# Optimization experiments

Hardware: AMD Instinct MI355X
Metric: run time of the kernel (lower is better)

## Reference

```python
import jax, jax.numpy as jnp
import numpy as np

H = 16  # num_attention_heads

def setup_inputs() -> dict:
    key = jax.random.key(0)
    ks = jax.random.split(key, 4)
    B, S, D = 4, 2048, 1024
    scale = 1.0 / np.sqrt(D)
    return {
        "hidden_states": jax.random.normal(ks[0], (B, S, D), dtype=jnp.float32),
        "attention_mask": jnp.zeros((B, 1, 1, S), dtype=jnp.float32),
        "Wq": jax.random.normal(ks[1], (D, D), dtype=jnp.float32) * scale,
        "bq": jnp.zeros((D,), dtype=jnp.float32),
        "Wk": jax.random.normal(ks[2], (D, D), dtype=jnp.float32) * scale,
        "bk": jnp.zeros((D,), dtype=jnp.float32),
        "Wv": jax.random.normal(ks[3], (D, D), dtype=jnp.float32) * scale,
        "bv": jnp.zeros((D,), dtype=jnp.float32),
    }

def _split_heads(x, B, S):
    # [B,S,D] -> [B,H,S,Dh]
    return x.reshape(B, S, H, -1).transpose(0, 2, 1, 3)

def reference(hidden_states, attention_mask, Wq, bq, Wk, bk, Wv, bv):
    B, S, D = hidden_states.shape
    Dh = D // H
    q = _split_heads(hidden_states @ Wq.T + bq, B, S)  # [B,H,S,Dh]
    k = _split_heads(hidden_states @ Wk.T + bk, B, S)
    v = _split_heads(hidden_states @ Wv.T + bv, B, S)
    scores = jnp.einsum("bhqd,bhkd->bhqk", q, k) / jnp.sqrt(jnp.float32(Dh))
    scores = scores + attention_mask  # additive mask, broadcast [B,1,1,S]
    probs = jax.nn.softmax(scores, axis=-1)  # dropout is identity in eval mode
    ctx = jnp.einsum("bhqk,bhkd->bhqd", probs, v)  # [B,H,S,Dh]
    ctx = ctx.transpose(0, 2, 1, 3).reshape(B, S, D)
    return ctx
```

## Files before the change

### kernel.cpp

```cpp
#include <hip/hip_runtime.h>
#include <hip/hip_bf16.h>
#include <stdint.h>

#define LOG2E 1.44269504088896340736f
#define SCL   (0.125f * LOG2E)

typedef __attribute__((ext_vector_type(8)))  short short8;
typedef __attribute__((ext_vector_type(16))) float floatx16;
typedef __attribute__((ext_vector_type(4)))  unsigned short ushort4v;

#define GLP(g, l)                                                              \
    __builtin_amdgcn_global_load_lds(                                          \
        (const __attribute__((address_space(1))) void*)(g),                    \
        (__attribute__((address_space(3))) void*)(l), 16, 0, 0)

#if __has_builtin(__builtin_amdgcn_exp2f)
#define EXP2(x) __builtin_amdgcn_exp2f(x)
#else
#define EXP2(x) exp2f(x)
#endif

static __device__ __forceinline__ unsigned short f2bf(float f) {
    union { float f; unsigned u; } v; v.f = f;
    unsigned r = v.u + 0x7FFFu + ((v.u >> 16) & 1u);
    return (unsigned short)(r >> 16);
}

static __device__ __forceinline__ unsigned pack2bf(float a, float b) {
    __hip_bfloat162 h = __float22bfloat162_rn(make_float2(a, b));
    union { __hip_bfloat162 h; unsigned u; } c; c.h = h; return c.u;
}

#define EXPPACK(dst, sv, base) do {                                            \
        float p0 = EXP2((sv)[(base) + 0]), p1 = EXP2((sv)[(base) + 1]);        \
        float p2 = EXP2((sv)[(base) + 2]), p3 = EXP2((sv)[(base) + 3]);        \
        float p4 = EXP2((sv)[(base) + 4]), p5 = EXP2((sv)[(base) + 5]);        \
        float p6 = EXP2((sv)[(base) + 6]), p7 = EXP2((sv)[(base) + 7]);        \
        dst.uu[0] = pack2bf(p0, p1); dst.uu[1] = pack2bf(p2, p3);              \
        dst.uu[2] = pack2bf(p4, p5); dst.uu[3] = pack2bf(p6, p7);              \
    } while (0)

__global__ __launch_bounds__(256) void cvt_all(const float* __restrict__ X,
                                               const float* __restrict__ Wq,
                                               const float* __restrict__ Wk,
                                               const float* __restrict__ Wv,
                                               const float* __restrict__ mask,
                                               unsigned short* __restrict__ xb,
                                               unsigned short* __restrict__ wb,
                                               float* __restrict__ maskl) {
    int i = blockIdx.x * 256 + threadIdx.x;
    if (i < 2097152) {
        float4 v = ((const float4*)X)[i];
        ushort4v o;
        o.x = f2bf(v.x); o.y = f2bf(v.y); o.z = f2bf(v.z); o.w = f2bf(v.w);
        ((ushort4v*)xb)[i] = o;
    } else if (i < 2883584) {
        int j = i - 2097152;
        const float* src; int k;
        if (j < 262144)      { src = Wq; k = j; }
        else if (j < 524288) { src = Wk; k = j - 262144; }
        else                 { src = Wv; k = j - 524288; }
        float4 v = ((const float4*)src)[k];
        ushort4v o;
        o.x = f2bf(v.x); o.y = f2bf(v.y); o.z = f2bf(v.z); o.w = f2bf(v.w);
        ((ushort4v*)wb)[j] = o;
    } else if (i < 2883584 + 2048) {
        int j = i - 2883584;
        float4 v = ((const float4*)mask)[j];
        ((float4*)maskl)[j] = make_float4(v.x * LOG2E, v.y * LOG2E,
                                          v.z * LOG2E, v.w * LOG2E);
    }
}

__global__ __launch_bounds__(512)
__attribute__((amdgpu_waves_per_eu(2, 2))) void qkv_gemm(
        const unsigned short* __restrict__ X,
        const unsigned short* __restrict__ W,
        const float* __restrict__ bq, const float* __restrict__ bk,
        const float* __restrict__ bv,
        unsigned short* __restrict__ Qf,
        unsigned short* __restrict__ Kf,
        unsigned short* __restrict__ Vt)
{
    __shared__ __align__(16) unsigned short AB[65536];

    const int tid  = threadIdx.x;
    const int lane = tid & 63;
    const int wv   = tid >> 6;
    const int q32  = lane & 31;
    const int hi   = lane >> 5;
    const int sw   = q32 & 7;
    const int mBase = blockIdx.x * 256;
    const int nBase = blockIdx.y * 256;
    const int wm = (wv >> 2) * 128;
    const int wn = (wv & 3) * 64;

    floatx16 acc[4][2];
#pragma unroll
    for (int mi = 0; mi < 4; ++mi) { acc[mi][0] = 0.0f; acc[mi][1] = 0.0f; }

    const int sr = lane >> 3;
    const int kc = (lane & 7) ^ sr;

    const unsigned short* aBase[4];
    const unsigned short* bBase[4];
#pragma unroll
    for (int ks = 0; ks < 4; ++ks) {
        const int cs = ((2 * ks + hi) ^ sw) * 8;
        aBase[ks] = AB + ((wv >> 2) * 16 + (q32 >> 3)) * 512 + sw * 64 + cs;
        bBase[ks] = AB + 32768 + ((wv & 3) * 8 + (q32 >> 3)) * 512 + sw * 64 + cs;
    }

    auto STAGE = [&](int kb, int so) {
#pragma unroll
        for (int r = 0; r < 4; ++r) {
            const int seg = r * 8 + wv;
            const int row = seg * 8 + sr;
            GLP(X + (size_t)(mBase + row) * 1024 + kb + kc * 8, AB + so + seg * 512);
            GLP(W + (size_t)(nBase + row) * 1024 + kb + kc * 8, AB + 32768 + so + seg * 512);
        }
    };

    STAGE(0, 0);
    asm volatile("s_waitcnt vmcnt(0)" ::: "memory");
    __builtin_amdgcn_s_barrier();

#pragma unroll 1
    for (int t = 0; t < 16; ++t) {
        const int so  = (t & 1) * 16384;
        if (t < 15) STAGE((t + 1) * 64, ((t + 1) & 1) * 16384);
        short8 bF[2][4];
#pragma unroll
        for (int ni = 0; ni < 2; ++ni)
#pragma unroll
            for (int ks = 0; ks < 4; ++ks)
                bF[ni][ks] = *(const short8*)(bBase[ks] + so + ni * 2048);
#pragma unroll
        for (int mi = 0; mi < 4; ++mi) {
            short8 aF[4];
#pragma unroll
            for (int ks = 0; ks < 4; ++ks)
                aF[ks] = *(const short8*)(aBase[ks] + so + mi * 2048);
#pragma unroll
            for (int ks = 0; ks < 4; ++ks) {
                acc[mi][0] = __builtin_amdgcn_mfma_f32_32x32x16_bf16(
                    aF[ks], bF[0][ks], acc[mi][0], 0, 0, 0);
                acc[mi][1] = __builtin_amdgcn_mfma_f32_32x32x16_bf16(
                    aF[ks], bF[1][ks], acc[mi][1], 0, 0, 0);
            }
        }
        asm volatile("s_waitcnt vmcnt(0) lgkmcnt(0)" ::: "memory");
        __builtin_amdgcn_s_barrier();
    }

    if (blockIdx.y < 8) {
        unsigned short* dst = (blockIdx.y < 4) ? Qf : Kf;
        const float* bias   = (blockIdx.y < 4) ? bq : bk;
        const float scl     = (blockIdx.y < 4) ? SCL : 1.0f;
        const int nb = nBase & 1023;
        float bj[2];
#pragma unroll
        for (int ni = 0; ni < 2; ++ni)
            bj[ni] = bias[nb + wn + ni * 32 + q32];
#pragma unroll 1
        for (int hh = 0; hh < 2; ++hh) {
            if ((wm >> 7) == hh) {
#pragma unroll
                for (int ni = 0; ni < 2; ++ni) {
                    const int col = wn + ni * 32 + q32;
#pragma unroll
                    for (int mi = 0; mi < 4; ++mi)
#pragma unroll
                        for (int g = 0; g < 4; ++g) {
                            const int row0 = mi * 32 + g * 8 + hi * 4;
#pragma unroll
                            for (int rr = 0; rr < 4; ++rr)
                                AB[(row0 + rr) * 264 + col] =
                                    f2bf((acc[mi][ni][g * 4 + rr] + bj[ni]) * scl);
                        }
                }
            }
            __syncthreads();
#pragma unroll
            for (int it = 0; it < 8; ++it) {
                const int row  = it * 16 + (tid >> 5);
                const int part = tid & 31;
                short8 v = *(const short8*)(AB + row * 264 + part * 8);
                *(short8*)(dst + (size_t)(mBase + hh * 128 + row) * 1024
                               + nb + part * 8) = v;
            }
            __syncthreads();
        }
    } else {
#pragma unroll
        for (int ni = 0; ni < 2; ++ni) {
            const int c = (nBase - 2048) + wn + ni * 32 + q32;
            const int h = c >> 6;
            const int d = c & 63;
            const float bias = bv[c];
#pragma unroll
            for (int mi = 0; mi < 4; ++mi)
#pragma unroll
                for (int g = 0; g < 4; ++g) {
                    const int m0 = mBase + wm + mi * 32 + g * 8 + hi * 4;
                    const int b  = m0 >> 11;
                    const int s0 = m0 & 2047;
                    const int sp = (s0 & ~12) | ((s0 & 4) << 1) | ((s0 & 8) >> 1);
                    ushort4v pv;
#pragma unroll
                    for (int rr = 0; rr < 4; ++rr)
                        pv[rr] = f2bf(acc[mi][ni][g * 4 + rr] + bias);
                    *(ushort4v*)(Vt + (size_t)((b * 16 + h) * 64 + d) * 2048 + sp) = pv;
                }
        }
    }
}

__global__ __launch_bounds__(256)
__attribute__((amdgpu_waves_per_eu(2, 2))) void attn_kernel(
        const unsigned short* __restrict__ Qf,
        const unsigned short* __restrict__ Kf,
        const unsigned short* __restrict__ VT,
        const float* __restrict__ maskl,
        float* __restrict__ out)
{
    __shared__ __align__(16) unsigned short Ksh[2 * 128 * 64];
    __shared__ __align__(16) unsigned short Vsh[2 * 64 * 128];
    __shared__ __align__(16) float Mall[2048];

    const int tid  = threadIdx.x;
    const int lane = tid & 63;
    const int wv   = tid >> 6;
    const int q32  = lane & 31;
    const int hi   = lane >> 5;
    const int bh   = blockIdx.x & 63;
    const int qt   = blockIdx.x >> 6;
    const int b    = bh >> 4;
    const int h    = bh & 15;
    const int q0   = qt * 256 + wv * 64;
    const int sw   = q32 & 7;

    short8 bQ0[4], bQ1[4];
#pragma unroll
    for (int ks = 0; ks < 4; ++ks) {
        bQ0[ks] = *(const short8*)(Qf + (size_t)(b * 2048 + q0 + q32) * 1024
                                      + h * 64 + ks * 16 + hi * 8);
        bQ1[ks] = *(const short8*)(Qf + (size_t)(b * 2048 + q0 + 32 + q32) * 1024
                                      + h * 64 + ks * 16 + hi * 8);
    }

    short8 ones;
#pragma unroll
    for (int j = 0; j < 8; ++j) ones[j] = (short)0x3F80;

    floatx16 accO00 = 0.0f, accO01 = 0.0f;
    floatx16 accO10 = 0.0f, accO11 = 0.0f;
    floatx16 lacc0 = 0.0f, lacc1 = 0.0f;

    const unsigned short* gK = Kf + (size_t)(b * 2048) * 1024 + h * 64;
    const unsigned short* gV = VT + (size_t)(bh * 64) * 2048;
    const float* mrow = maskl + b * 2048;

    const unsigned short* kb4[4];
    const unsigned short* vb4[4];
#pragma unroll
    for (int ks = 0; ks < 4; ++ks) {
        const int cs = (2 * ks + hi) ^ sw;
        kb4[ks] = Ksh + q32 * 64 + cs * 8;
        vb4[ks] = Vsh + q32 * 128 + cs * 8;
    }

    const int krr = lane >> 3;
    const int kcs = lane & 7;
    const int vrr = lane >> 4;
    const int vcs = lane & 15;

    auto STAGE = [&](int kbn, int so) {
#pragma unroll
        for (int s = 0; s < 4; ++s) {
            const int seg = wv * 4 + s;
            const int rK  = seg * 8 + krr;
            const int cK  = kcs ^ (rK & 7);
            GLP(gK + (size_t)(kbn + rK) * 1024 + cK * 8, Ksh + so + seg * 512);
            const int rV  = seg * 4 + vrr;
            const int cV  = vcs ^ (rV & 7);
            GLP(gV + (size_t)rV * 2048 + kbn + cV * 8, Vsh + so + seg * 512);
        }
    };

    auto TILE = [&](int kb, int ro, int so) {
        if (kb + 128 < 2048) STAGE(kb + 128, so);
        const float* mloc = Mall + kb + hi * 4;
#pragma unroll 1
        for (int half = 0; half < 2; ++half) {
            short8 aK0[4], aK1[4];
#pragma unroll
            for (int ks = 0; ks < 4; ++ks) {
                aK0[ks] = *(const short8*)(kb4[ks] + ro + half * 4096);
                aK1[ks] = *(const short8*)(kb4[ks] + ro + half * 4096 + 2048);
            }
            const float* mh = mloc + half * 64;
#pragma unroll
            for (int mt = 0; mt < 2; ++mt) {
                const short8* aK = (mt == 0) ? aK0 : aK1;
                floatx16 mC;
#pragma unroll
                for (int a = 0; a < 4; ++a) {
                    float4 mv = *(const float4*)(mh + mt * 32 + a * 8);
                    mC[4 * a + 0] = mv.x; mC[4 * a + 1] = mv.y;
                    mC[4 * a + 2] = mv.z; mC[4 * a + 3] = mv.w;
                }
                __builtin_amdgcn_s_setprio(1);
                floatx16 s0 = __builtin_amdgcn_mfma_f32_32x32x16_bf16(aK[0], bQ0[0], mC, 0, 0, 0);
                floatx16 s1 = __builtin_amdgcn_mfma_f32_32x32x16_bf16(aK[0], bQ1[0], mC, 0, 0, 0);
#pragma unroll
                for (int ks = 1; ks < 4; ++ks) {
                    s0 = __builtin_amdgcn_mfma_f32_32x32x16_bf16(aK[ks], bQ0[ks], s0, 0, 0, 0);
                    s1 = __builtin_amdgcn_mfma_f32_32x32x16_bf16(aK[ks], bQ1[ks], s1, 0, 0, 0);
                }
                __builtin_amdgcn_s_setprio(0);
                short8 bVa0 = *(const short8*)(vb4[2 * mt + 0] + ro + half * 64);
                short8 bVa1 = *(const short8*)(vb4[2 * mt + 0] + ro + 4096 + half * 64);
                short8 bVb0 = *(const short8*)(vb4[2 * mt + 1] + ro + half * 64);
                short8 bVb1 = *(const short8*)(vb4[2 * mt + 1] + ro + 4096 + half * 64);
                union { unsigned uu[4]; short8 s; } aPa, aPb, aPc, aPd;
                EXPPACK(aPa, s0, 0);
                EXPPACK(aPb, s0, 8);
                EXPPACK(aPc, s1, 0);
                EXPPACK(aPd, s1, 8);
                __builtin_amdgcn_s_setprio(1);
                accO00 = __builtin_amdgcn_mfma_f32_32x32x16_bf16(aPa.s, bVa0, accO00, 0, 0, 0);
                accO01 = __builtin_amdgcn_mfma_f32_32x32x16_bf16(aPa.s, bVa1, accO01, 0, 0, 0);
                lacc0  = __builtin_amdgcn_mfma_f32_32x32x16_bf16(aPa.s, ones, lacc0, 0, 0, 0);
                accO00 = __builtin_amdgcn_mfma_f32_32x32x16_bf16(aPb.s, bVb0, accO00, 0, 0, 0);
                accO01 = __builtin_amdgcn_mfma_f32_32x32x16_bf16(aPb.s, bVb1, accO01, 0, 0, 0);
                lacc0  = __builtin_amdgcn_mfma_f32_32x32x16_bf16(aPb.s, ones, lacc0, 0, 0, 0);
                accO10 = __builtin_amdgcn_mfma_f32_32x32x16_bf16(aPc.s, bVa0, accO10, 0, 0, 0);
                accO11 = __builtin_amdgcn_mfma_f32_32x32x16_bf16(aPc.s, bVa1, accO11, 0, 0, 0);
                lacc1  = __builtin_amdgcn_mfma_f32_32x32x16_bf16(aPc.s, ones, lacc1, 0, 0, 0);
                accO10 = __builtin_amdgcn_mfma_f32_32x32x16_bf16(aPd.s, bVb0, accO10, 0, 0, 0);
                accO11 = __builtin_amdgcn_mfma_f32_32x32x16_bf16(aPd.s, bVb1, accO11, 0, 0, 0);
                lacc1  = __builtin_amdgcn_mfma_f32_32x32x16_bf16(aPd.s, ones, lacc1, 0, 0, 0);
                __builtin_amdgcn_s_setprio(0);
            }
        }
        asm volatile("s_waitcnt vmcnt(0) lgkmcnt(0)" ::: "memory");
        __builtin_amdgcn_s_barrier();
    };

#pragma unroll
    for (int s = 0; s < 2; ++s)
        GLP(mrow + (wv * 2 + s) * 256 + lane * 4, Mall + (wv * 2 + s) * 256);
    STAGE(0, 0);
    asm volatile("s_waitcnt vmcnt(0)" ::: "memory");
    __builtin_amdgcn_s_barrier();

#pragma unroll 1
    for (int kb2 = 0; kb2 < 2048; kb2 += 256) {
        TILE(kb2,       0,    8192);
        TILE(kb2 + 128, 8192, 0);
    }

#pragma unroll
    for (int g = 0; g < 4; ++g)
#pragma unroll
        for (int rr = 0; rr < 4; ++rr) {
            const int r   = g * 4 + rr;
            const int row = rr + 8 * g + 4 * hi;
            const float li0 = 1.0f / lacc0[r];
            const float li1 = 1.0f / lacc1[r];
            float* op0 = out + (size_t)(b * 2048 + q0 + row) * 1024 + h * 64 + q32;
            float* op1 = out + (size_t)(b * 2048 + q0 + 32 + row) * 1024 + h * 64 + q32;
            op0[0]  = accO00[r] * li0;
            op0[32] = accO01[r] * li0;
            op1[0]  = accO10[r] * li1;
            op1[32] = accO11[r] * li1;
        }
}

extern "C" void kernel_launch(void* const* d_in, const int* in_sizes, int n_in,
                              void* d_out, int out_size, void* d_ws, size_t ws_size,
                              hipStream_t stream) {
    const float* X    = (const float*)d_in[0];
    const float* mask = (const float*)d_in[1];
    const float* Wq   = (const float*)d_in[2];
    const float* bq   = (const float*)d_in[3];
    const float* Wk   = (const float*)d_in[4];
    const float* bk   = (const float*)d_in[5];
    const float* Wv   = (const float*)d_in[6];
    const float* bv   = (const float*)d_in[7];
    float* out = (float*)d_out;

    char* ws = (char*)d_ws;
    unsigned short* xb  = (unsigned short*)(ws);
    unsigned short* wb  = (unsigned short*)(ws + 16777216);
    unsigned short* qf  = (unsigned short*)(ws + 23068672);
    unsigned short* kf  = (unsigned short*)(ws + 39845888);
    unsigned short* vtb = (unsigned short*)(ws + 56623104);
    float*          ml  = (float*)(ws + 73400320);

    cvt_all<<<11272, 256, 0, stream>>>(X, Wq, Wk, Wv, mask, xb, wb, ml);

    qkv_gemm<<<dim3(32, 12), 512, 0, stream>>>(xb, wb, bq, bk, bv, qf, kf, vtb);

    attn_kernel<<<512, 256, 0, stream>>>(qf, kf, vtb, ml, out);
}
```

Before: 243.8 us.

## Software-pipeline QK MFMAs with exp and compute row sums on VALU

The attention inner tile is restructured into four phases. Each phase issues the QK^T MFMAs for the next 32-key subtile while exponentiating and packing the current scores, so matrix-core work overlaps the exp/pack VALU work. Row sums are now accumulated in fp32 on the VALU from the exponentials, then reduced across half-waves with a shuffle and passed through LDS. This replaces the extra MFMAs against a ones vector, removing a third of the PV-stage MFMAs. The cost is more live registers for the double-buffered score tiles and a normaliser summed from unrounded fp32 values instead of the bf16 values fed to the PV product.

After: 407.1 us. 1.67x slower.

```diff
diff --git a/kernel.cpp b/kernel.cpp
--- a/kernel.cpp
+++ b/kernel.cpp
@@ -31,11 +31,12 @@
     union { __hip_bfloat162 h; unsigned u; } c; c.h = h; return c.u;
 }
 
-#define EXPPACK(dst, sv, base) do {                                            \
+#define EXPPACKL(dst, sv, base, lacc) do {                                     \
         float p0 = EXP2((sv)[(base) + 0]), p1 = EXP2((sv)[(base) + 1]);        \
         float p2 = EXP2((sv)[(base) + 2]), p3 = EXP2((sv)[(base) + 3]);        \
         float p4 = EXP2((sv)[(base) + 4]), p5 = EXP2((sv)[(base) + 5]);        \
         float p6 = EXP2((sv)[(base) + 6]), p7 = EXP2((sv)[(base) + 7]);        \
+        lacc += ((p0 + p1) + (p2 + p3)) + ((p4 + p5) + (p6 + p7));             \
         dst.uu[0] = pack2bf(p0, p1); dst.uu[1] = pack2bf(p2, p3);              \
         dst.uu[2] = pack2bf(p4, p5); dst.uu[3] = pack2bf(p6, p7);              \
     } while (0)
@@ -227,6 +228,7 @@
     __shared__ __align__(16) unsigned short Ksh[2 * 128 * 64];
     __shared__ __align__(16) unsigned short Vsh[2 * 64 * 128];
     __shared__ __align__(16) float Mall[2048];
+    __shared__ __align__(16) float Lsh[256];
 
     const int tid  = threadIdx.x;
     const int lane = tid & 63;
@@ -249,13 +251,9 @@
                                       + h * 64 + ks * 16 + hi * 8);
     }
 
-    short8 ones;
-#pragma unroll
-    for (int j = 0; j < 8; ++j) ones[j] = (short)0x3F80;
-
     floatx16 accO00 = 0.0f, accO01 = 0.0f;
     floatx16 accO10 = 0.0f, accO11 = 0.0f;
-    floatx16 lacc0 = 0.0f, lacc1 = 0.0f;
+    float l0 = 0.0f, l1 = 0.0f;
 
     const unsigned short* gK = Kf + (size_t)(b * 2048) * 1024 + h * 64;
     const unsigned short* gV = VT + (size_t)(bh * 64) * 2048;
@@ -288,62 +286,77 @@
         }
     };
 
+    auto SREAD = [&](int t4, int ro, const float* mloc, short8 aK[4], floatx16& mC) {
+        const int half = t4 >> 1, mt = t4 & 1;
+#pragma unroll
+        for (int ks = 0; ks < 4; ++ks)
+            aK[ks] = *(const short8*)(kb4[ks] + ro + half * 4096 + mt * 2048);
+        const float* mh = mloc + half * 64 + mt * 32;
+#pragma unroll
+        for (int a = 0; a < 4; ++a) {
+            float4 mv = *(const float4*)(mh + a * 8);
+            mC[4 * a + 0] = mv.x; mC[4 * a + 1] = mv.y;
+            mC[4 * a + 2] = mv.z; mC[4 * a + 3] = mv.w;
+        }
+    };
+
+    auto SMFMA = [&](const short8 aK[4], const floatx16& mC,
+                     floatx16& s0, floatx16& s1) {
+        __builtin_amdgcn_s_setprio(1);
+        s0 = __builtin_amdgcn_mfma_f32_32x32x16_bf16(aK[0], bQ0[0], mC, 0, 0, 0);
+        s1 = __builtin_amdgcn_mfma_f32_32x32x16_bf16(aK[0], bQ1[0], mC, 0, 0, 0);
+#pragma unroll
+        for (int ks = 1; ks < 4; ++ks) {
+            s0 = __builtin_amdgcn_mfma_f32_32x32x16_bf16(aK[ks], bQ0[ks], s0, 0, 0, 0);
+            s1 = __builtin_amdgcn_mfma_f32_32x32x16_bf16(aK[ks], bQ1[ks], s1, 0, 0, 0);
+        }
+        __builtin_amdgcn_s_setprio(0);
+    };
+
+    auto PHASE = [&](int cur, int ro, const float* mloc, bool readNext,
+                     floatx16& sc0, floatx16& sc1, floatx16& sn0, floatx16& sn1) {
+        const int half = cur >> 1, mt = cur & 1;
+        short8 aKn[4]; floatx16 mCn;
+        if (readNext) SREAD(cur + 1, ro, mloc, aKn, mCn);
+        union { unsigned uu[4]; short8 s; } aPa, aPb, aPc, aPd;
+        EXPPACKL(aPa, sc0, 0, l0);
+        EXPPACKL(aPb, sc0, 8, l0);
+        short8 bVa0 = *(const short8*)(vb4[2 * mt + 0] + ro + half * 64);
+        short8 bVa1 = *(const short8*)(vb4[2 * mt + 0] + ro + 4096 + half * 64);
+        short8 bVb0 = *(const short8*)(vb4[2 * mt + 1] + ro + half * 64);
+        short8 bVb1 = *(const short8*)(vb4[2 * mt + 1] + ro + 4096 + half * 64);
+        if (readNext) SMFMA(aKn, mCn, sn0, sn1);
+        EXPPACKL(aPc, sc1, 0, l1);
+        EXPPACKL(aPd, sc1, 8, l1);
+        __builtin_amdgcn_s_setprio(1);
+        accO00 = __builtin_amdgcn_mfma_f32_32x32x16_bf16(aPa.s, bVa0, accO00, 0, 0, 0);
+        accO01 = __builtin_amdgcn_mfma_f32_32x32x16_bf16(aPa.s, bVa1, accO01, 0, 0, 0);
+        accO00 = __builtin_amdgcn_mfma_f32_32x32x16_bf16(aPb.s, bVb0, accO00, 0, 0, 0);
+        accO01 = __builtin_amdgcn_mfma_f32_32x32x16_bf16(aPb.s, bVb1, accO01, 0, 0, 0);
+        accO10 = __builtin_amdgcn_mfma_f32_32x32x16_bf16(aPc.s, bVa0, accO10, 0, 0, 0);
+        accO11 = __builtin_amdgcn_mfma_f32_32x32x16_bf16(aPc.s, bVa1, accO11, 0, 0, 0);
+        accO10 = __builtin_amdgcn_mfma_f32_32x32x16_bf16(aPd.s, bVb0, accO10, 0, 0, 0);
+        accO11 = __builtin_amdgcn_mfma_f32_32x32x16_bf16(aPd.s, bVb1, accO11, 0, 0, 0);
+        __builtin_amdgcn_s_setprio(0);
+    };
+
     auto TILE = [&](int kb, int ro, int so) {
         if (kb + 128 < 2048) STAGE(kb + 128, so);
         const float* mloc = Mall + kb + hi * 4;
-#pragma unroll 1
-        for (int half = 0; half < 2; ++half) {
-            short8 aK0[4], aK1[4];
-#pragma unroll
-            for (int ks = 0; ks < 4; ++ks) {
-                aK0[ks] = *(const short8*)(kb4[ks] + ro + half * 4096);
-                aK1[ks] = *(const short8*)(kb4[ks] + ro + half * 4096 + 2048);
-            }
-            const float* mh = mloc + half * 64;
-#pragma unroll
-            for (int mt = 0; mt < 2; ++mt) {
-                const short8* aK = (mt == 0) ? aK0 : aK1;
-                floatx16 mC;
-#pragma unroll
-                for (int a = 0; a < 4; ++a) {
-                    float4 mv = *(const float4*)(mh + mt * 32 + a * 8);
-                    mC[4 * a + 0] = mv.x; mC[4 * a + 1] = mv.y;
-                    mC[4 * a + 2] = mv.z; mC[4 * a + 3] = mv.w;
-                }
-                __builtin_amdgcn_s_setprio(1);
-                floatx16 s0 = __builtin_amdgcn_mfma_f32_32x32x16_bf16(aK[0], bQ0[0], mC, 0, 0, 0);
-                floatx16 s1 = __builtin_amdgcn_mfma_f32_32x32x16_bf16(aK[0], bQ1[0], mC, 0, 0, 0);
-#pragma unroll
-                for (int ks = 1; ks < 4; ++ks) {
-                    s0 = __builtin_amdgcn_mfma_f32_32x32x16_bf16(aK[ks], bQ0[ks], s0, 0, 0, 0);
-                    s1 = __builtin_amdgcn_mfma_f32_32x32x16_bf16(aK[ks], bQ1[ks], s1, 0, 0, 0);
-                }
-                __builtin_amdgcn_s_setprio(0);
-                short8 bVa0 = *(const short8*)(vb4[2 * mt + 0] + ro + half * 64);
-                short8 bVa1 = *(const short8*)(vb4[2 * mt + 0] + ro + 4096 + half * 64);
-                short8 bVb0 = *(const short8*)(vb4[2 * mt + 1] + ro + half * 64);
-                short8 bVb1 = *(const short8*)(vb4[2 * mt + 1] + ro + 4096 + half * 64);
-                union { unsigned uu[4]; short8 s; } aPa, aPb, aPc, aPd;
-                EXPPACK(aPa, s0, 0);
-                EXPPACK(aPb, s0, 8);
-                EXPPACK(aPc, s1, 0);
-                EXPPACK(aPd, s1, 8);
-                __builtin_amdgcn_s_setprio(1);
-                accO00 = __builtin_amdgcn_mfma_f32_32x32x16_bf16(aPa.s, bVa0, accO00, 0, 0, 0);
-                accO01 = __builtin_amdgcn_mfma_f32_32x32x16_bf16(aPa.s, bVa1, accO01, 0, 0, 0);
-                lacc0  = __builtin_amdgcn_mfma_f32_32x32x16_bf16(aPa.s, ones, lacc0, 0, 0, 0);
-                accO00 = __builtin_amdgcn_mfma_f32_32x32x16_bf16(aPb.s, bVb0, accO00, 0, 0, 0);
-                accO01 = __builtin_amdgcn_mfma_f32_32x32x16_bf16(aPb.s, bVb1, accO01, 0, 0, 0);
-                lacc0  = __builtin_amdgcn_mfma_f32_32x32x16_bf16(aPb.s, ones, lacc0, 0, 0, 0);
-                accO10 = __builtin_amdgcn_mfma_f32_32x32x16_bf16(aPc.s, bVa0, accO10, 0, 0, 0);
-                accO11 = __builtin_amdgcn_mfma_f32_32x32x16_bf16(aPc.s, bVa1, accO11, 0, 0, 0);
-                lacc1  = __builtin_amdgcn_mfma_f32_32x32x16_bf16(aPc.s, ones, lacc1, 0, 0, 0);
-                accO10 = __builtin_amdgcn_mfma_f32_32x32x16_bf16(aPd.s, bVb0, accO10, 0, 0, 0);
-                accO11 = __builtin_amdgcn_mfma_f32_32x32x16_bf16(aPd.s, bVb1, accO11, 0, 0, 0);
-                lacc1  = __builtin_amdgcn_mfma_f32_32x32x16_bf16(aPd.s, ones, lacc1, 0, 0, 0);
-                __builtin_amdgcn_s_setprio(0);
-            }
-        }
+        floatx16 sA0, sA1, sB0, sB1;
+        {
+            short8 aK[4]; floatx16 mC;
+            SREAD(0, ro, mloc, aK, mC);
+            SMFMA(aK, mC, sA0, sA1);
+        }
+        __builtin_amdgcn_sched_barrier(0);
+        PHASE(0, ro, mloc, true,  sA0, sA1, sB0, sB1);
+        __builtin_amdgcn_sched_barrier(0);
+        PHASE(1, ro, mloc, true,  sB0, sB1, sA0, sA1);
+        __builtin_amdgcn_sched_barrier(0);
+        PHASE(2, ro, mloc, true,  sA0, sA1, sB0, sB1);
+        __builtin_amdgcn_sched_barrier(0);
+        PHASE(3, ro, mloc, false, sB0, sB1, sA0, sA1);
         asm volatile("s_waitcnt vmcnt(0) lgkmcnt(0)" ::: "memory");
         __builtin_amdgcn_s_barrier();
     };
@@ -361,21 +374,32 @@
         TILE(kb2 + 128, 8192, 0);
     }
 
-#pragma unroll
-    for (int g = 0; g < 4; ++g)
+    l0 += __shfl_xor(l0, 32, 64);
+    l1 += __shfl_xor(l1, 32, 64);
+    if (lane < 32) {
+        Lsh[wv * 64 + q32]      = 1.0f / l0;
+        Lsh[wv * 64 + 32 + q32] = 1.0f / l1;
+    }
+#pragma unroll
+    for (int g = 0; g < 4; ++g) {
+        float4 i0 = *(const float4*)(Lsh + wv * 64 + g * 8 + hi * 4);
+        float4 i1 = *(const float4*)(Lsh + wv * 64 + 32 + g * 8 + hi * 4);
 #pragma unroll
         for (int rr = 0; rr < 4; ++rr) {
             const int r   = g * 4 + rr;
             const int row = rr + 8 * g + 4 * hi;
-            const float li0 = 1.0f / lacc0[r];
-            const float li1 = 1.0f / lacc1[r];
+            const float l0v = (rr == 0) ? i0.x : (rr == 1) ? i0.y
+                            : (rr == 2) ? i0.z : i0.w;
+            const float l1v = (rr == 0) ? i1.x : (rr == 1) ? i1.y
+                            : (rr == 2) ? i1.z : i1.w;
             float* op0 = out + (size_t)(b * 2048 + q0 + row) * 1024 + h * 64 + q32;
             float* op1 = out + (size_t)(b * 2048 + q0 + 32 + row) * 1024 + h * 64 + q32;
-            op0[0]  = accO00[r] * li0;
-            op0[32] = accO01[r] * li0;
-            op1[0]  = accO10[r] * li1;
-            op1[32] = accO11[r] * li1;
-        }
+            op0[0]  = accO00[r] * l0v;
+            op0[32] = accO01[r] * l0v;
+            op1[0]  = accO10[r] * l1v;
+            op1[32] = accO11[r] * l1v;
+        }
+    }
 }
 
 extern "C" void kernel_launch(void* const* d_in, const int* in_sizes, int n_in,
```
